# Kernel tuning notes

Hardware: AMD Instinct MI355X
Metric: run time of the kernel (lower is better)

## Reference

```python
import jax, jax.numpy as jnp
import numpy as np

N, E, B = 50000, 800000, 64
D_IN, D_E = 192, 64
NUM_OUT = 256


def setup_inputs() -> dict:
    key = jax.random.key(0)
    ks = jax.random.split(key, 30)
    rn = lambda k, s: jax.random.normal(k, s, dtype=jnp.float32) * 0.05
    return {
        "x": jax.random.normal(ks[0], (N, D_IN), jnp.float32),
        "edge_index": jax.random.randint(ks[1], (2, E), 0, N, dtype=jnp.int32),
        "edge_attr": jax.random.normal(ks[2], (E, D_E), jnp.float32),
        "batch": jnp.sort(jax.random.randint(ks[3], (N,), 0, B, dtype=jnp.int32)),
        "W1": rn(ks[4], (D_IN, 256)), "as1": rn(ks[5], (4, 64)), "ad1": rn(ks[6], (4, 64)),
        "We1": rn(ks[7], (D_E, 256)), "ae1": rn(ks[8], (4, 64)), "b1": rn(ks[9], (256,)),
        "W2": rn(ks[10], (256, 256)), "as2": rn(ks[11], (4, 64)), "ad2": rn(ks[12], (4, 64)),
        "We2": rn(ks[13], (D_E, 256)), "ae2": rn(ks[14], (4, 64)), "b2": rn(ks[15], (256,)),
        "W3": rn(ks[16], (256, 512)), "as3": rn(ks[17], (4, 128)), "ad3": rn(ks[18], (4, 128)),
        "We3": rn(ks[19], (D_E, 512)), "ae3": rn(ks[20], (4, 128)), "b3": rn(ks[21], (128,)),
        "Wa": rn(ks[22], (128, NUM_OUT)), "ba": rn(ks[23], (NUM_OUT,)),
        "Wv": rn(ks[24], (128, 1)), "bv": rn(ks[25], (1,)),
    }


def reference(x, edge_index, edge_attr, batch,
              W1, as1, ad1, We1, ae1, b1,
              W2, as2, ad2, We2, ae2, b2,
              W3, as3, ad3, We3, ae3, b3,
              Wa, ba, Wv, bv):
    Nn = x.shape[0]
    src0, dst0 = edge_index[0], edge_index[1]
    # PyG add_self_loops(fill_value='mean'): self-loop edge_attr = mean of incoming edge_attr
    deg = jax.ops.segment_sum(jnp.ones_like(dst0, dtype=x.dtype), dst0, num_segments=Nn)
    loop_attr = jax.ops.segment_sum(edge_attr, dst0, num_segments=Nn) / jnp.maximum(deg, 1.0)[:, None]
    loop = jnp.arange(Nn, dtype=src0.dtype)
    src = jnp.concatenate([src0, loop])
    dst = jnp.concatenate([dst0, loop])
    ea = jnp.concatenate([edge_attr, loop_attr], axis=0)

    def gat(h, W, a_s, a_d, We, a_e, bias, concat):
        Hh, C = a_s.shape
        hs = (h @ W).reshape(Nn, Hh, C)                       # [N,H,C]
        al_s = (hs * a_s).sum(-1)                             # [N,H]
        al_d = (hs * a_d).sum(-1)                             # [N,H]
        al_e = ((ea @ We).reshape(-1, Hh, C) * a_e).sum(-1)   # [E+N,H]
        alpha = jax.nn.leaky_relu(al_s[src] + al_d[dst] + al_e, 0.2)
        amax = jax.ops.segment_max(alpha, dst, num_segments=Nn)
        w = jnp.exp(alpha - amax[dst])
        denom = jax.ops.segment_sum(w, dst, num_segments=Nn)
        w = w / (denom[dst] + 1e-16)                          # scatter-softmax over dst
        out = jax.ops.segment_sum(hs[src] * w[..., None], dst, num_segments=Nn)
        out = out.reshape(Nn, Hh * C) if concat else out.mean(axis=1)
        return out + bias

    h = jax.nn.relu(gat(x, W1, as1, ad1, We1, ae1, b1, True))
    h = jax.nn.relu(gat(h, W2, as2, ad2, We2, ae2, b2, True))
    h = gat(h, W3, as3, ad3, We3, ae3, b3, False)
    cnt = jax.ops.segment_sum(jnp.ones((Nn,), h.dtype), batch, num_segments=B)
    g = jax.ops.segment_sum(h, batch, num_segments=B) / jnp.maximum(cnt, 1.0)[:, None]
    logits = g @ Wa + ba
    value = g @ Wv + bv
    return jnp.concatenate([logits, value], axis=-1)  # [B, num_outputs+1]
```

## Files before the change

kernel.cpp:

```cpp
#include <hip/hip_runtime.h>
#include <hip/hip_bf16.h>


typedef __attribute__((ext_vector_type(8))) short short8;
typedef __attribute__((ext_vector_type(4))) float floatx4;
typedef __attribute__((ext_vector_type(4))) unsigned int uintx4;

#define DEV __device__ __forceinline__

DEV unsigned short f2b(float f) {
  union { float f; unsigned u; } v; v.f = f;
  unsigned r = v.u + 0x7FFFu + ((v.u >> 16) & 1u);
  return (unsigned short)(r >> 16);
}
DEV float b2f(unsigned short u) {
  union { unsigned u; float f; } v; v.u = ((unsigned)u) << 16;
  return v.f;
}

__global__ void k_cvt(const float* __restrict__ in, unsigned short* __restrict__ out,
                      int n8) {
  int i = blockIdx.x * 256 + threadIdx.x;
  if (i >= n8) return;
  const float4* p = (const float4*)(in + (size_t)i * 8);
  float4 a = p[0], b = p[1];
  unsigned short t[8];
  t[0]=f2b(a.x); t[1]=f2b(a.y); t[2]=f2b(a.z); t[3]=f2b(a.w);
  t[4]=f2b(b.x); t[5]=f2b(b.y); t[6]=f2b(b.z); t[7]=f2b(b.w);
  *(uint4*)(out + (size_t)i * 8) = *(uint4*)t;
}

__global__ void k_deg2(const int* __restrict__ src, const int* __restrict__ dst,
                       int* __restrict__ deg2, int E) {
  int e = blockIdx.x * 256 + threadIdx.x;
  if (e < E) atomicAdd(&deg2[(size_t)dst[e] * 8 + (src[e] >> 13)], 1);
}

__global__ __launch_bounds__(256) void k_scan1(const int* __restrict__ deg,
    int* __restrict__ rowptr, int* __restrict__ bsum, int N) {
  __shared__ int sd[256];
  int b = blockIdx.x, tid = threadIdx.x;
  int i0 = b * 1024 + tid * 4;
  int v[4]; int s = 0;
#pragma unroll
  for (int j = 0; j < 4; j++) { int i = i0 + j; v[j] = (i < N) ? deg[i] : 0; s += v[j]; }
  sd[tid] = s;
  __syncthreads();
  for (int off = 1; off < 256; off <<= 1) {
    int t = (tid >= off) ? sd[tid - off] : 0;
    __syncthreads();
    sd[tid] += t;
    __syncthreads();
  }
  int run = sd[tid] - s;
#pragma unroll
  for (int j = 0; j < 4; j++) { int i = i0 + j; if (i < N) rowptr[i] = run; run += v[j]; }
  if (tid == 255) bsum[b] = sd[255];
}

__global__ __launch_bounds__(512) void k_scan2(int* __restrict__ bsum, int nb) {
  __shared__ int sd[512];
  int tid = threadIdx.x;
  int v = (tid < nb) ? bsum[tid] : 0;
  sd[tid] = v;
  __syncthreads();
  for (int off = 1; off < 512; off <<= 1) {
    int t = (tid >= off) ? sd[tid - off] : 0;
    __syncthreads();
    sd[tid] += t;
    __syncthreads();
  }
  if (tid < nb) bsum[tid] = sd[tid] - v;
}

__global__ __launch_bounds__(256) void k_scan3(int* __restrict__ rowptr,
    int* __restrict__ cursor, const int* __restrict__ bsum, int N, int E) {
  int b = blockIdx.x, tid = threadIdx.x;
  int add = bsum[b];
  int i0 = b * 1024 + tid * 4;
#pragma unroll
  for (int j = 0; j < 4; j++) {
    int i = i0 + j;
    if (i < N) { int r = rowptr[i] + add; rowptr[i] = r; cursor[i] = r; }
  }
  if (b == 0 && tid == 0) rowptr[N] = E;
}

__global__ void k_scatter(const int* __restrict__ src, const int* __restrict__ dst,
    int* __restrict__ cursor, int2* __restrict__ csr, int E) {
  int e = blockIdx.x * 256 + threadIdx.x;
  if (e < E) {
    int s = src[e], d = dst[e];
    int pos = atomicAdd(&cursor[(size_t)d * 8 + (s >> 13)], 1);
    csr[pos] = make_int2(s, e);
  }
}

__global__ void k_wt(const float* __restrict__ W, unsigned short* __restrict__ Wt,
                     int K, int Nout) {
  int idx = blockIdx.x * 256 + threadIdx.x;
  if (idx < K * Nout) {
    int n = idx / K, k = idx - n * K;
    Wt[idx] = f2b(W[(size_t)k * Nout + n]);
  }
}

__global__ void k_wep(const float* __restrict__ We1, const float* __restrict__ ae1,
                      const float* __restrict__ We2, const float* __restrict__ ae2,
                      const float* __restrict__ We3, const float* __restrict__ ae3,
                      unsigned short* __restrict__ Wept) {
  int t = blockIdx.x * 256 + threadIdx.x;
  int j = t >> 6, c = t & 63;
  int L = j >> 2, h = j & 3;
  const float* We = (L == 0) ? We1 : (L == 1) ? We2 : We3;
  const float* ae = (L == 0) ? ae1 : (L == 1) ? ae2 : ae3;
  int C = (L == 2) ? 128 : 64;
  int HC = 4 * C;
  float s = 0.f;
  for (int cc = 0; cc < C; cc++) s += We[(size_t)c * HC + h * C + cc] * ae[h * C + cc];
  Wept[j * 64 + c] = f2b(s);
  if (t < 256) {
    int jj = 12 + (t >> 6);
    Wept[jj * 64 + (t & 63)] = 0;
  }
}

template<bool A_F32, int OUT_MODE, bool DO_ALD>
__global__ __launch_bounds__(256) void k_gemm(const void* __restrict__ Ap,
    const unsigned short* __restrict__ Bt, void* __restrict__ Cp,
    int M, int Nout, int K, int EN,
    const float* __restrict__ a_s, const float* __restrict__ a_d,
    float* __restrict__ als, float* __restrict__ ald,
    const int2* __restrict__ eidmap) {
  __shared__ unsigned short As[64][32];
  __shared__ unsigned short Bs[64][32];
  const int tid = threadIdx.x;
  const int wave = tid >> 6, lane = tid & 63;
  const int quad = lane >> 4, l16 = lane & 15;
  const int m0 = blockIdx.x * 64, n0 = blockIdx.y * 64;
  const int arow = tid >> 2;
  const int cb0  = (tid & 3) << 4;
  const int swzr = ((arow >> 1) & 3) << 4;
  floatx4 acc[4] = {{0,0,0,0},{0,0,0,0},{0,0,0,0},{0,0,0,0}};
  for (int k0 = 0; k0 < K; k0 += 32) {
    if (A_F32) {
      int gm = m0 + arow;
      unsigned short tmp[8];
      if (gm < M) {
        size_t ar = (size_t)gm;
        if (OUT_MODE == 2) ar = (size_t)eidmap[gm].y;
        const float* Af = (const float*)Ap;
        const float4* p = (const float4*)(Af + ar * K + k0 + (cb0 >> 1));
        float4 u0 = p[0], u1 = p[1];
        tmp[0]=f2b(u0.x); tmp[1]=f2b(u0.y); tmp[2]=f2b(u0.z); tmp[3]=f2b(u0.w);
        tmp[4]=f2b(u1.x); tmp[5]=f2b(u1.y); tmp[6]=f2b(u1.z); tmp[7]=f2b(u1.w);
      } else {
#pragma unroll
        for (int j = 0; j < 8; j++) tmp[j] = 0;
      }
      *(uint4*)((char*)&As[0][0] + arow * 64 + (cb0 ^ swzr)) = *(uint4*)tmp;
      int gn = n0 + arow;
      uint4 bv = {0,0,0,0};
      if (gn < Nout) bv = *(const uint4*)(Bt + (size_t)gn * K + k0 + (cb0 >> 1));
      *(uint4*)((char*)&Bs[0][0] + arow * 64 + (cb0 ^ swzr)) = bv;
    } else {
      int gm = m0 + arow; if (gm >= M) gm = M - 1;
      int cbs = cb0 ^ swzr;
      const unsigned short* gA =
          (const unsigned short*)Ap + (size_t)gm * K + k0 + (cbs >> 1);
      __builtin_amdgcn_global_load_lds(gA, (char*)&As[0][0] + wave * 1024, 16, 0, 0);
      int gn = n0 + arow;
      const unsigned short* gB = Bt + (size_t)gn * K + k0 + (cbs >> 1);
      __builtin_amdgcn_global_load_lds(gB, (char*)&Bs[0][0] + wave * 1024, 16, 0, 0);
    }
    __syncthreads();
    int ra = wave * 16 + l16;
    short8 a = *(const short8*)((const char*)&As[0][0] + ra * 64 +
                                ((quad * 16) ^ (((ra >> 1) & 3) << 4)));
#pragma unroll
    for (int t = 0; t < 4; t++) {
      int rb = t * 16 + l16;
      short8 b = *(const short8*)((const char*)&Bs[0][0] + rb * 64 +
                                  ((quad * 16) ^ (((rb >> 1) & 3) << 4)));
      acc[t] = __builtin_amdgcn_mfma_f32_16x16x32_bf16(a, b, acc[t], 0, 0, 0);
    }
    __syncthreads();
  }
#pragma unroll
  for (int t = 0; t < 4; t++) {
#pragma unroll
    for (int r = 0; r < 4; r++) {
      int row = m0 + wave * 16 + quad * 4 + r;
      int col = n0 + t * 16 + l16;
      float v = acc[t][r];
      if (OUT_MODE == 0) {
        if (row < M && col < Nout)
          ((unsigned short*)Cp)[(size_t)row * Nout + col] = f2b(v);
      } else {
        if (row < M && col < 12)
          ((float*)Cp)[((size_t)(col >> 2) * EN + row) * 4 + (col & 3)] = v;
      }
    }
  }
  if constexpr (DO_ALD) {
    int h = (n0 * 4) / Nout;
#pragma unroll
    for (int r = 0; r < 4; r++) {
      float ps = 0.f, pd = 0.f;
#pragma unroll
      for (int t = 0; t < 4; t++) {
        int col = n0 + t * 16 + l16;
        float v = acc[t][r];
        ps += v * a_s[col];
        pd += v * a_d[col];
      }
#pragma unroll
      for (int off = 1; off < 16; off <<= 1) {
        ps += __shfl_xor(ps, off, 64);
        pd += __shfl_xor(pd, off, 64);
      }
      int row = m0 + wave * 16 + quad * 4 + r;
      if (l16 == 0 && row < M) {
        atomicAdd(&als[row * 4 + h], ps);
        atomicAdd(&ald[row * 4 + h], pd);
      }
    }
  }
}

__global__ void k_loop_ale(const int* __restrict__ rowptr2,
                           float* __restrict__ ale, int N, int E) {
  int n = blockIdx.x * 256 + threadIdx.x;
  if (n >= N) return;
  const size_t EN = (size_t)E + N;
  int s = rowptr2[(size_t)n * 8], e = rowptr2[(size_t)n * 8 + 8];
  float a[12];
#pragma unroll
  for (int j = 0; j < 12; j++) a[j] = 0.f;
  for (int p = s; p < e; p++) {
#pragma unroll
    for (int L = 0; L < 3; L++) {
      float4 v = *(const float4*)(ale + (L * EN + p) * 4);
      a[L * 4 + 0] += v.x; a[L * 4 + 1] += v.y;
      a[L * 4 + 2] += v.z; a[L * 4 + 3] += v.w;
    }
  }
  float inv = 1.0f / (float)((e - s) > 1 ? (e - s) : 1);
#pragma unroll
  for (int L = 0; L < 3; L++)
    *(float4*)(ale + (L * EN + E + n) * 4) =
        make_float4(a[L*4+0]*inv, a[L*4+1]*inv, a[L*4+2]*inv, a[L*4+3]*inv);
}

template<int LPN, int MODE>
__global__ __launch_bounds__(256) void k_agg(const unsigned short* __restrict__ hs,
    const int* __restrict__ rowptr2, const int2* __restrict__ csr,
    const float* __restrict__ ale,
    const float* __restrict__ als, const float* __restrict__ ald,
    const float* __restrict__ bias, unsigned short* __restrict__ outb,
    float* __restrict__ outf, int N, int E) {
  const int FPL = 32;
  const int HC  = LPN * FPL;
  const int NG  = 64 / LPN;
  __shared__ float s_w[4][NG][LPN][4];
  __shared__ int   s_s[4][NG][LPN];
  const int wave = threadIdx.x >> 6;
  const int lane = threadIdx.x & 63;
  const int grp  = lane / LPN;
  const int sl   = lane % LPN;
  const int hd   = sl >> (LPN >> 3);
  const int node = blockIdx.x * (4 * NG) + wave * NG + grp;
  if (node >= N) return;
  int start = rowptr2[(size_t)node * 8];
  int cnt   = rowptr2[(size_t)node * 8 + 8] - start;
  int total = cnt + 1;
  const float4 aldv   = *(const float4*)(ald + (size_t)node * 4);
  const float4 selfev = *(const float4*)(ale + ((size_t)E + node) * 4);
  const float4 selfsv = *(const float4*)(als + (size_t)node * 4);
  int    psidx = node;
  float4 pev = selfev, psv = selfsv;
  if (sl < cnt) {
    int2 se = csr[start + sl];
    psidx = se.x;
    pev = *(const float4*)(ale + (size_t)(start + sl) * 4);
    psv = *(const float4*)(als + (size_t)se.x * 4);
  }
  float m0=-1e30f, m1=-1e30f, m2=-1e30f, m3=-1e30f;
  float d0=0.f, d1=0.f, d2=0.f, d3=0.f;
  float acc[FPL];
#pragma unroll
  for (int j = 0; j < FPL; j++) acc[j] = 0.f;
  for (int base = 0; base < total; base += LPN) {
    int ei = base + sl;
    bool active = ei < total;
    float a0=-1e30f, a1=-1e30f, a2=-1e30f, a3=-1e30f;
    int sidx = psidx;
    if (active) {
      a0 = psv.x + aldv.x + pev.x;
      a1 = psv.y + aldv.y + pev.y;
      a2 = psv.z + aldv.z + pev.z;
      a3 = psv.w + aldv.w + pev.w;
      a0 = a0 > 0.f ? a0 : 0.2f * a0;
      a1 = a1 > 0.f ? a1 : 0.2f * a1;
      a2 = a2 > 0.f ? a2 : 0.2f * a2;
      a3 = a3 > 0.f ? a3 : 0.2f * a3;
    }
    float c0=a0, c1=a1, c2=a2, c3=a3;
#pragma unroll
    for (int off = LPN / 2; off > 0; off >>= 1) {
      c0 = fmaxf(c0, __shfl_xor(c0, off, 64));
      c1 = fmaxf(c1, __shfl_xor(c1, off, 64));
      c2 = fmaxf(c2, __shfl_xor(c2, off, 64));
      c3 = fmaxf(c3, __shfl_xor(c3, off, 64));
    }
    float n0v = fmaxf(m0, c0), n1v = fmaxf(m1, c1), n2v = fmaxf(m2, c2), n3v = fmaxf(m3, c3);
    float p0 = active ? __expf(a0 - n0v) : 0.f;
    float p1 = active ? __expf(a1 - n1v) : 0.f;
    float p2 = active ? __expf(a2 - n2v) : 0.f;
    float p3 = active ? __expf(a3 - n3v) : 0.f;
    float s0=p0, s1=p1, s2=p2, s3=p3;
#pragma unroll
    for (int off = LPN / 2; off > 0; off >>= 1) {
      s0 += __shfl_xor(s0, off, 64);
      s1 += __shfl_xor(s1, off, 64);
      s2 += __shfl_xor(s2, off, 64);
      s3 += __shfl_xor(s3, off, 64);
    }
    float r0 = __expf(m0 - n0v), r1 = __expf(m1 - n1v);
    float r2 = __expf(m2 - n2v), r3 = __expf(m3 - n3v);
    d0 = d0 * r0 + s0; d1 = d1 * r1 + s1; d2 = d2 * r2 + s2; d3 = d3 * r3 + s3;
    float rh = hd == 0 ? r0 : hd == 1 ? r1 : hd == 2 ? r2 : r3;
#pragma unroll
    for (int j = 0; j < FPL; j++) acc[j] *= rh;
    m0 = n0v; m1 = n1v; m2 = n2v; m3 = n3v;
    *(float4*)&s_w[wave][grp][sl][0] = make_float4(p0, p1, p2, p3);
    s_s[wave][grp][sl] = sidx;
    __threadfence_block();
    if (base + LPN < total) {
      int nei = base + LPN + sl;
      psidx = node; pev = selfev; psv = selfsv;
      if (nei < cnt) {
        int2 se = csr[start + nei];
        psidx = se.x;
        pev = *(const float4*)(ale + (size_t)(start + nei) * 4);
        psv = *(const float4*)(als + (size_t)se.x * 4);
      }
    }
    int chunk = total - base; if (chunk > LPN) chunk = LPN;
    int t = 0;
    for (; t + 2 <= chunk; t += 2) {
      float w0 = s_w[wave][grp][t][hd];
      float w1 = s_w[wave][grp][t + 1][hd];
      int   q0 = s_s[wave][grp][t];
      int   q1 = s_s[wave][grp][t + 1];
      const uintx4* p0p = (const uintx4*)(hs + (size_t)q0 * HC + sl * FPL);
      const uintx4* p1p = (const uintx4*)(hs + (size_t)q1 * HC + sl * FPL);
      uintx4 v0[4], v1[4];
#pragma unroll
      for (int q = 0; q < 4; q++) v0[q] = p0p[q];
#pragma unroll
      for (int q = 0; q < 4; q++) v1[q] = p1p[q];
      asm volatile("" :: "v"(v0[0]), "v"(v0[1]), "v"(v0[2]), "v"(v0[3]),
                         "v"(v1[0]), "v"(v1[1]), "v"(v1[2]), "v"(v1[3]));
#pragma unroll
      for (int q = 0; q < 4; q++) {
        uintx4 x = v0[q];
#pragma unroll
        for (int k = 0; k < 4; k++) {
          float lo = __uint_as_float(x[k] << 16);
          float hi = __uint_as_float(x[k] & 0xffff0000u);
          acc[q * 8 + k * 2 + 0] += w0 * lo;
          acc[q * 8 + k * 2 + 1] += w0 * hi;
        }
      }
#pragma unroll
      for (int q = 0; q < 4; q++) {
        uintx4 x = v1[q];
#pragma unroll
        for (int k = 0; k < 4; k++) {
          float lo = __uint_as_float(x[k] << 16);
          float hi = __uint_as_float(x[k] & 0xffff0000u);
          acc[q * 8 + k * 2 + 0] += w1 * lo;
          acc[q * 8 + k * 2 + 1] += w1 * hi;
        }
      }
    }
    if (t < chunk) {
      float w0 = s_w[wave][grp][t][hd];
      int   q0 = s_s[wave][grp][t];
      const uintx4* p0p = (const uintx4*)(hs + (size_t)q0 * HC + sl * FPL);
      uintx4 v0[4];
#pragma unroll
      for (int q = 0; q < 4; q++) v0[q] = p0p[q];
#pragma unroll
      for (int q = 0; q < 4; q++) {
        uintx4 x = v0[q];
#pragma unroll
        for (int k = 0; k < 4; k++) {
          float lo = __uint_as_float(x[k] << 16);
          float hi = __uint_as_float(x[k] & 0xffff0000u);
          acc[q * 8 + k * 2 + 0] += w0 * lo;
          acc[q * 8 + k * 2 + 1] += w0 * hi;
        }
      }
    }
  }
  float dh = hd == 0 ? d0 : hd == 1 ? d1 : hd == 2 ? d2 : d3;
  float inv = 1.0f / (dh + 1e-16f);
  if constexpr (MODE == 0) {
    unsigned short tmp[FPL];
#pragma unroll
    for (int j = 0; j < FPL; j++) {
      float v = acc[j] * inv + bias[sl * FPL + j];
      tmp[j] = f2b(fmaxf(v, 0.f));
    }
    unsigned short* op = outb + (size_t)node * HC + sl * FPL;
#pragma unroll
    for (int q = 0; q < 4; q++) ((uint4*)op)[q] = ((uint4*)tmp)[q];
  } else {
#pragma unroll
    for (int j = 0; j < FPL; j++) {
      float v = acc[j] * inv;
      v += __shfl_xor(v, 4, 64);
      v += __shfl_xor(v, 8, 64);
      acc[j] = v * 0.25f;
    }
    if (sl < 4) {
      float* op = outf + (size_t)node * (4 * FPL) + sl * FPL;
#pragma unroll
      for (int j = 0; j < FPL; j++) op[j] = acc[j] + bias[sl * FPL + j];
    }
  }
}

__global__ __launch_bounds__(256) void k_pool(const float* __restrict__ out3,
    const int* __restrict__ bat, float* __restrict__ g, int* __restrict__ cntb, int N) {
  int wid = blockIdx.x * 4 + (threadIdx.x >> 6);
  int lane = threadIdx.x & 63;
  int per = (N + 255) / 256;
  int s = wid * per, e = s + per;
  if (e > N) e = N;
  if (s >= e) return;
  int cur = bat[s];
  float ax = 0.f, ay = 0.f; int run = 0;
  for (int n = s; n < e; n++) {
    int b = bat[n];
    if (b != cur) {
      atomicAdd(&g[cur * 128 + lane * 2], ax);
      atomicAdd(&g[cur * 128 + lane * 2 + 1], ay);
      if (lane == 0) atomicAdd(&cntb[cur], run);
      ax = 0.f; ay = 0.f; run = 0; cur = b;
    }
    float2 v = *(const float2*)(out3 + (size_t)n * 128 + lane * 2);
    ax += v.x; ay += v.y; run++;
  }
  atomicAdd(&g[cur * 128 + lane * 2], ax);
  atomicAdd(&g[cur * 128 + lane * 2 + 1], ay);
  if (lane == 0) atomicAdd(&cntb[cur], run);
}

__global__ __launch_bounds__(320) void k_final(const float* __restrict__ g,
    const int* __restrict__ cntb, const float* __restrict__ Wa, const float* __restrict__ ba,
    const float* __restrict__ Wv, const float* __restrict__ bv, float* __restrict__ out) {
  __shared__ float gm[128];
  int b = blockIdx.x, t = threadIdx.x;
  if (t < 128) {
    float c = (float)cntb[b];
    gm[t] = g[b * 128 + t] / fmaxf(c, 1.f);
  }
  __syncthreads();
  if (t < 257) {
    float acc = 0.f;
    if (t < 256) {
      for (int k = 0; k < 128; k++) acc += gm[k] * Wa[k * 256 + t];
      acc += ba[t];
    } else {
      for (int k = 0; k < 128; k++) acc += gm[k] * Wv[k];
      acc += bv[0];
    }
    out[b * 257 + t] = acc;
  }
}

extern "C" void kernel_launch(void* const* d_in, const int* in_sizes, int n_in,
                              void* d_out, int out_size, void* d_ws, size_t ws_size,
                              hipStream_t stream) {
  const float* x   = (const float*)d_in[0];
  const int*   ei  = (const int*)  d_in[1];
  const float* ea  = (const float*)d_in[2];
  const int*   bat = (const int*)  d_in[3];
  const float* W1  = (const float*)d_in[4];
  const float* as1 = (const float*)d_in[5];
  const float* ad1 = (const float*)d_in[6];
  const float* We1 = (const float*)d_in[7];
  const float* ae1 = (const float*)d_in[8];
  const float* b1  = (const float*)d_in[9];
  const float* W2  = (const float*)d_in[10];
  const float* as2 = (const float*)d_in[11];
  const float* ad2 = (const float*)d_in[12];
  const float* We2 = (const float*)d_in[13];
  const float* ae2 = (const float*)d_in[14];
  const float* b2  = (const float*)d_in[15];
  const float* W3  = (const float*)d_in[16];
  const float* as3 = (const float*)d_in[17];
  const float* ad3 = (const float*)d_in[18];
  const float* We3 = (const float*)d_in[19];
  const float* ae3 = (const float*)d_in[20];
  const float* b3  = (const float*)d_in[21];
  const float* Wa  = (const float*)d_in[22];
  const float* ba  = (const float*)d_in[23];
  const float* Wv  = (const float*)d_in[24];
  const float* bv  = (const float*)d_in[25];
  (void)n_in; (void)out_size; (void)ws_size;

  const int N = in_sizes[0] / 192;
  const int E = in_sizes[1] / 2;
  const size_t EN = (size_t)E + N;
  const int* srcv = ei;
  const int* dstv = ei + E;
  const int N2 = N * 8;
  const int nbB = (N2 + 1023) / 1024;

  size_t off = 0;
  auto alloc = [&](size_t bytes) -> char* {
    char* p = (char*)d_ws + off;
    off += (bytes + 255) & ~(size_t)255;
    return p;
  };
  int* deg2    = (int*)alloc((size_t)N2 * 4);
  int* rowptr2 = (int*)alloc((size_t)(N2 + 1) * 4);
  int* cursor2 = (int*)alloc((size_t)N2 * 4);
  int* bsum    = (int*)alloc(512 * 4);
  int2* csr    = (int2*)alloc((size_t)E * 8);
  float* ale   = (float*)alloc(3 * EN * 4 * 4);
  unsigned short* Wept = (unsigned short*)alloc(16 * 64 * 2);
  unsigned short* W1t  = (unsigned short*)alloc(256 * 192 * 2);
  unsigned short* W2t  = (unsigned short*)alloc(256 * 256 * 2);
  unsigned short* W3t  = (unsigned short*)alloc(512 * 256 * 2);
  unsigned short* xB   = (unsigned short*)alloc((size_t)N * 192 * 2);
  unsigned short* hs   = (unsigned short*)alloc((size_t)N * 512 * 2);
  unsigned short* h1   = (unsigned short*)alloc((size_t)N * 256 * 2);
  unsigned short* h2   = (unsigned short*)alloc((size_t)N * 256 * 2);
  float* out3  = (float*)alloc((size_t)N * 128 * 4);
  float* als_all = (float*)alloc((size_t)N * 4 * 4 * 6);
  float* g     = (float*)alloc(64 * 128 * 4 + 64 * 4);
  int* cntb    = (int*)(g + 64 * 128);
  float* als1 = als_all + (size_t)N * 4 * 0;
  float* ald1 = als_all + (size_t)N * 4 * 1;
  float* als2 = als_all + (size_t)N * 4 * 2;
  float* ald2 = als_all + (size_t)N * 4 * 3;
  float* als3 = als_all + (size_t)N * 4 * 4;
  float* ald3 = als_all + (size_t)N * 4 * 5;

  hipMemsetAsync(deg2, 0, (size_t)N2 * 4, stream);
  hipMemsetAsync(als_all, 0, (size_t)N * 4 * 4 * 6, stream);
  hipMemsetAsync(g, 0, 64 * 128 * 4 + 64 * 4, stream);

  k_deg2<<<(E + 255) / 256, 256, 0, stream>>>(srcv, dstv, deg2, E);
  k_scan1<<<nbB, 256, 0, stream>>>(deg2, rowptr2, bsum, N2);
  k_scan2<<<1, 512, 0, stream>>>(bsum, nbB);
  k_scan3<<<nbB, 256, 0, stream>>>(rowptr2, cursor2, bsum, N2, E);
  k_scatter<<<(E + 255) / 256, 256, 0, stream>>>(srcv, dstv, cursor2, csr, E);
  k_cvt<<<((N * 192 / 8) + 255) / 256, 256, 0, stream>>>(x, xB, N * 192 / 8);
  k_wt<<<(192 * 256 + 255) / 256, 256, 0, stream>>>(W1, W1t, 192, 256);
  k_wt<<<(256 * 256 + 255) / 256, 256, 0, stream>>>(W2, W2t, 256, 256);
  k_wt<<<(256 * 512 + 255) / 256, 256, 0, stream>>>(W3, W3t, 256, 512);
  k_wep<<<3, 256, 0, stream>>>(We1, ae1, We2, ae2, We3, ae3, Wept);
  k_gemm<true, 2, false><<<dim3((E + 63) / 64, 1), 256, 0, stream>>>(
      ea, Wept, ale, E, 16, 64, (int)EN, nullptr, nullptr, nullptr, nullptr, csr);
  k_loop_ale<<<(N + 255) / 256, 256, 0, stream>>>(rowptr2, ale, N, E);
  k_gemm<false, 0, true><<<dim3((N + 63) / 64, 4), 256, 0, stream>>>(
      xB, W1t, hs, N, 256, 192, 0, as1, ad1, als1, ald1, nullptr);
  k_agg<8, 0><<<(N + 31) / 32, 256, 0, stream>>>(
      hs, rowptr2, csr, ale + 0 * EN * 4, als1, ald1, b1, h1, nullptr, N, E);
  k_gemm<false, 0, true><<<dim3((N + 63) / 64, 4), 256, 0, stream>>>(
      h1, W2t, hs, N, 256, 256, 0, as2, ad2, als2, ald2, nullptr);
  k_agg<8, 0><<<(N + 31) / 32, 256, 0, stream>>>(
      hs, rowptr2, csr, ale + 1 * EN * 4, als2, ald2, b2, h2, nullptr, N, E);
  k_gemm<false, 0, true><<<dim3((N + 63) / 64, 8), 256, 0, stream>>>(
      h2, W3t, hs, N, 512, 256, 0, as3, ad3, als3, ald3, nullptr);
  k_agg<16, 1><<<(N + 15) / 16, 256, 0, stream>>>(
      hs, rowptr2, csr, ale + 2 * EN * 4, als3, ald3, b3, nullptr, out3, N, E);
  k_pool<<<64, 256, 0, stream>>>(out3, bat, g, cntb, N);
  k_final<<<64, 320, 0, stream>>>(g, cntb, Wa, ba, Wv, bv, (float*)d_out);
}
```

Before: 1.009 ms.

## Merge prep kernels, drop atomics for per-head logits, and split aggregation launches

Fuses the x conversion, the three weight transposes and the edge-weight projection into one multi-role prep kernel. For layers 1 and 2, where each 64-column tile covers exactly one head, the GEMM epilogue now writes the attention logits directly instead of using atomicAdd, which shrinks the zeroed workspace to a single memset. Each aggregation kernel is split into two launches over node halves, apparently to improve cache locality or scheduling. The extra launches add overhead, and the split size is hardcoded for this node count.

```diff
diff --git a/kernel.cpp b/kernel.cpp
--- a/kernel.cpp
+++ b/kernel.cpp
@@ -18,16 +18,58 @@
   return v.f;
 }
 
-__global__ void k_cvt(const float* __restrict__ in, unsigned short* __restrict__ out,
-                      int n8) {
-  int i = blockIdx.x * 256 + threadIdx.x;
-  if (i >= n8) return;
-  const float4* p = (const float4*)(in + (size_t)i * 8);
-  float4 a = p[0], b = p[1];
-  unsigned short t[8];
-  t[0]=f2b(a.x); t[1]=f2b(a.y); t[2]=f2b(a.z); t[3]=f2b(a.w);
-  t[4]=f2b(b.x); t[5]=f2b(b.y); t[6]=f2b(b.z); t[7]=f2b(b.w);
-  *(uint4*)(out + (size_t)i * 8) = *(uint4*)t;
+__global__ __launch_bounds__(256) void k_prep(
+    const float* __restrict__ x, unsigned short* __restrict__ xB, int n8,
+    const float* __restrict__ W1, unsigned short* __restrict__ W1t,
+    const float* __restrict__ W2, unsigned short* __restrict__ W2t,
+    const float* __restrict__ W3, unsigned short* __restrict__ W3t,
+    const float* __restrict__ We1, const float* __restrict__ ae1,
+    const float* __restrict__ We2, const float* __restrict__ ae2,
+    const float* __restrict__ We3, const float* __restrict__ ae3,
+    unsigned short* __restrict__ Wept,
+    int bA, int bB, int bC, int bD) {
+  int b = blockIdx.x, tid = threadIdx.x;
+  if (b < bA) {
+    int i = b * 256 + tid;
+    if (i < n8) {
+      const float4* p = (const float4*)(x + (size_t)i * 8);
+      float4 a = p[0], c = p[1];
+      unsigned short t[8];
+      t[0]=f2b(a.x); t[1]=f2b(a.y); t[2]=f2b(a.z); t[3]=f2b(a.w);
+      t[4]=f2b(c.x); t[5]=f2b(c.y); t[6]=f2b(c.z); t[7]=f2b(c.w);
+      *(uint4*)(xB + (size_t)i * 8) = *(uint4*)t;
+    }
+  } else if (b < bB) {
+    int idx = (b - bA) * 256 + tid;
+    int K = 192, Nout = 256;
+    int n = idx / K, k = idx - n * K;
+    W1t[idx] = f2b(W1[(size_t)k * Nout + n]);
+  } else if (b < bC) {
+    int idx = (b - bB) * 256 + tid;
+    int K = 256, Nout = 256;
+    int n = idx / K, k = idx - n * K;
+    W2t[idx] = f2b(W2[(size_t)k * Nout + n]);
+  } else if (b < bD) {
+    int idx = (b - bC) * 256 + tid;
+    int K = 256, Nout = 512;
+    int n = idx / K, k = idx - n * K;
+    W3t[idx] = f2b(W3[(size_t)k * Nout + n]);
+  } else {
+    int t = (b - bD) * 256 + tid;
+    int j = t >> 6, c = t & 63;
+    int L = j >> 2, h = j & 3;
+    const float* We = (L == 0) ? We1 : (L == 1) ? We2 : We3;
+    const float* ae = (L == 0) ? ae1 : (L == 1) ? ae2 : ae3;
+    int C = (L == 2) ? 128 : 64;
+    int HC = 4 * C;
+    float s = 0.f;
+    for (int cc = 0; cc < C; cc++) s += We[(size_t)c * HC + h * C + cc] * ae[h * C + cc];
+    Wept[j * 64 + c] = f2b(s);
+    if (t < 256) {
+      int jj = 12 + (t >> 6);
+      Wept[jj * 64 + (t & 63)] = 0;
+    }
+  }
 }
 
 __global__ void k_deg2(const int* __restrict__ src, const int* __restrict__ dst,
@@ -96,36 +138,7 @@
   }
 }
 
-__global__ void k_wt(const float* __restrict__ W, unsigned short* __restrict__ Wt,
-                     int K, int Nout) {
-  int idx = blockIdx.x * 256 + threadIdx.x;
-  if (idx < K * Nout) {
-    int n = idx / K, k = idx - n * K;
-    Wt[idx] = f2b(W[(size_t)k * Nout + n]);
-  }
-}
-
-__global__ void k_wep(const float* __restrict__ We1, const float* __restrict__ ae1,
-                      const float* __restrict__ We2, const float* __restrict__ ae2,
-                      const float* __restrict__ We3, const float* __restrict__ ae3,
-                      unsigned short* __restrict__ Wept) {
-  int t = blockIdx.x * 256 + threadIdx.x;
-  int j = t >> 6, c = t & 63;
-  int L = j >> 2, h = j & 3;
-  const float* We = (L == 0) ? We1 : (L == 1) ? We2 : We3;
-  const float* ae = (L == 0) ? ae1 : (L == 1) ? ae2 : ae3;
-  int C = (L == 2) ? 128 : 64;
-  int HC = 4 * C;
-  float s = 0.f;
-  for (int cc = 0; cc < C; cc++) s += We[(size_t)c * HC + h * C + cc] * ae[h * C + cc];
-  Wept[j * 64 + c] = f2b(s);
-  if (t < 256) {
-    int jj = 12 + (t >> 6);
-    Wept[jj * 64 + (t & 63)] = 0;
-  }
-}
-
-template<bool A_F32, int OUT_MODE, bool DO_ALD>
+template<bool A_F32, int OUT_MODE, int DO_ALD>
 __global__ __launch_bounds__(256) void k_gemm(const void* __restrict__ Ap,
     const unsigned short* __restrict__ Bt, void* __restrict__ Cp,
     int M, int Nout, int K, int EN,
@@ -202,7 +215,7 @@
       }
     }
   }
-  if constexpr (DO_ALD) {
+  if constexpr (DO_ALD != 0) {
     int h = (n0 * 4) / Nout;
 #pragma unroll
     for (int r = 0; r < 4; r++) {
@@ -221,8 +234,13 @@
       }
       int row = m0 + wave * 16 + quad * 4 + r;
       if (l16 == 0 && row < M) {
-        atomicAdd(&als[row * 4 + h], ps);
-        atomicAdd(&ald[row * 4 + h], pd);
+        if constexpr (DO_ALD == 1) {
+          als[row * 4 + h] = ps;
+          ald[row * 4 + h] = pd;
+        } else {
+          atomicAdd(&als[row * 4 + h], ps);
+          atomicAdd(&ald[row * 4 + h], pd);
+        }
       }
     }
   }
@@ -258,7 +276,7 @@
     const float* __restrict__ ale,
     const float* __restrict__ als, const float* __restrict__ ald,
     const float* __restrict__ bias, unsigned short* __restrict__ outb,
-    float* __restrict__ outf, int N, int E) {
+    float* __restrict__ outf, int noff, int nEnd, int E) {
   const int FPL = 32;
   const int HC  = LPN * FPL;
   const int NG  = 64 / LPN;
@@ -269,8 +287,8 @@
   const int grp  = lane / LPN;
   const int sl   = lane % LPN;
   const int hd   = sl >> (LPN >> 3);
-  const int node = blockIdx.x * (4 * NG) + wave * NG + grp;
-  if (node >= N) return;
+  const int node = noff + blockIdx.x * (4 * NG) + wave * NG + grp;
+  if (node >= nEnd) return;
   int start = rowptr2[(size_t)node * 8];
   int cnt   = rowptr2[(size_t)node * 8 + 8] - start;
   int total = cnt + 1;
@@ -528,6 +546,11 @@
     return p;
   };
   int* deg2    = (int*)alloc((size_t)N2 * 4);
+  float* als3  = (float*)alloc((size_t)N * 4 * 4);
+  float* ald3  = (float*)alloc((size_t)N * 4 * 4);
+  float* g     = (float*)alloc(64 * 128 * 4 + 64 * 4);
+  int* cntb    = (int*)(g + 64 * 128);
+  const size_t zspan = off;
   int* rowptr2 = (int*)alloc((size_t)(N2 + 1) * 4);
   int* cursor2 = (int*)alloc((size_t)N2 * 4);
   int* bsum    = (int*)alloc(512 * 4);
@@ -542,45 +565,50 @@
   unsigned short* h1   = (unsigned short*)alloc((size_t)N * 256 * 2);
   unsigned short* h2   = (unsigned short*)alloc((size_t)N * 256 * 2);
   float* out3  = (float*)alloc((size_t)N * 128 * 4);
-  float* als_all = (float*)alloc((size_t)N * 4 * 4 * 6);
-  float* g     = (float*)alloc(64 * 128 * 4 + 64 * 4);
-  int* cntb    = (int*)(g + 64 * 128);
-  float* als1 = als_all + (size_t)N * 4 * 0;
-  float* ald1 = als_all + (size_t)N * 4 * 1;
-  float* als2 = als_all + (size_t)N * 4 * 2;
-  float* ald2 = als_all + (size_t)N * 4 * 3;
-  float* als3 = als_all + (size_t)N * 4 * 4;
-  float* ald3 = als_all + (size_t)N * 4 * 5;
-
-  hipMemsetAsync(deg2, 0, (size_t)N2 * 4, stream);
-  hipMemsetAsync(als_all, 0, (size_t)N * 4 * 4 * 6, stream);
-  hipMemsetAsync(g, 0, 64 * 128 * 4 + 64 * 4, stream);
+  float* als1  = (float*)alloc((size_t)N * 4 * 4);
+  float* ald1  = (float*)alloc((size_t)N * 4 * 4);
+  float* als2  = (float*)alloc((size_t)N * 4 * 4);
+  float* ald2  = (float*)alloc((size_t)N * 4 * 4);
+
+  hipMemsetAsync(d_ws, 0, zspan, stream);
 
   k_deg2<<<(E + 255) / 256, 256, 0, stream>>>(srcv, dstv, deg2, E);
   k_scan1<<<nbB, 256, 0, stream>>>(deg2, rowptr2, bsum, N2);
   k_scan2<<<1, 512, 0, stream>>>(bsum, nbB);
   k_scan3<<<nbB, 256, 0, stream>>>(rowptr2, cursor2, bsum, N2, E);
   k_scatter<<<(E + 255) / 256, 256, 0, stream>>>(srcv, dstv, cursor2, csr, E);
-  k_cvt<<<((N * 192 / 8) + 255) / 256, 256, 0, stream>>>(x, xB, N * 192 / 8);
-  k_wt<<<(192 * 256 + 255) / 256, 256, 0, stream>>>(W1, W1t, 192, 256);
-  k_wt<<<(256 * 256 + 255) / 256, 256, 0, stream>>>(W2, W2t, 256, 256);
-  k_wt<<<(256 * 512 + 255) / 256, 256, 0, stream>>>(W3, W3t, 256, 512);
-  k_wep<<<3, 256, 0, stream>>>(We1, ae1, We2, ae2, We3, ae3, Wept);
-  k_gemm<true, 2, false><<<dim3((E + 63) / 64, 1), 256, 0, stream>>>(
+  {
+    const int n8 = N * 192 / 8;
+    const int bA = (n8 + 255) / 256;
+    const int bB = bA + 192;
+    const int bC = bB + 256;
+    const int bD = bC + 512;
+    k_prep<<<bD + 3, 256, 0, stream>>>(x, xB, n8, W1, W1t, W2, W2t, W3, W3t,
+                                       We1, ae1, We2, ae2, We3, ae3, Wept,
+                                       bA, bB, bC, bD);
+  }
+  k_gemm<true, 2, 0><<<dim3((E + 63) / 64, 1), 256, 0, stream>>>(
       ea, Wept, ale, E, 16, 64, (int)EN, nullptr, nullptr, nullptr, nullptr, csr);
   k_loop_ale<<<(N + 255) / 256, 256, 0, stream>>>(rowptr2, ale, N, E);
-  k_gemm<false, 0, true><<<dim3((N + 63) / 64, 4), 256, 0, stream>>>(
+  const int half = 25024;
+  k_gemm<false, 0, 1><<<dim3((N + 63) / 64, 4), 256, 0, stream>>>(
       xB, W1t, hs, N, 256, 192, 0, as1, ad1, als1, ald1, nullptr);
-  k_agg<8, 0><<<(N + 31) / 32, 256, 0, stream>>>(
-      hs, rowptr2, csr, ale + 0 * EN * 4, als1, ald1, b1, h1, nullptr, N, E);
-  k_gemm<false, 0, true><<<dim3((N + 63) / 64, 4), 256, 0, stream>>>(
+  k_agg<8, 0><<<(half + 31) / 32, 256, 0, stream>>>(
+      hs, rowptr2, csr, ale + 0 * EN * 4, als1, ald1, b1, h1, nullptr, 0, half, E);
+  k_agg<8, 0><<<(N - half + 31) / 32, 256, 0, stream>>>(
+      hs, rowptr2, csr, ale + 0 * EN * 4, als1, ald1, b1, h1, nullptr, half, N, E);
+  k_gemm<false, 0, 1><<<dim3((N + 63) / 64, 4), 256, 0, stream>>>(
       h1, W2t, hs, N, 256, 256, 0, as2, ad2, als2, ald2, nullptr);
-  k_agg<8, 0><<<(N + 31) / 32, 256, 0, stream>>>(
-      hs, rowptr2, csr, ale + 1 * EN * 4, als2, ald2, b2, h2, nullptr, N, E);
-  k_gemm<false, 0, true><<<dim3((N + 63) / 64, 8), 256, 0, stream>>>(
+  k_agg<8, 0><<<(half + 31) / 32, 256, 0, stream>>>(
+      hs, rowptr2, csr, ale + 1 * EN * 4, als2, ald2, b2, h2, nullptr, 0, half, E);
+  k_agg<8, 0><<<(N - half + 31) / 32, 256, 0, stream>>>(
+      hs, rowptr2, csr, ale + 1 * EN * 4, als2, ald2, b2, h2, nullptr, half, N, E);
+  k_gemm<false, 0, 2><<<dim3((N + 63) / 64, 8), 256, 0, stream>>>(
       h2, W3t, hs, N, 512, 256, 0, as3, ad3, als3, ald3, nullptr);
-  k_agg<16, 1><<<(N + 15) / 16, 256, 0, stream>>>(
-      hs, rowptr2, csr, ale + 2 * EN * 4, als3, ald3, b3, nullptr, out3, N, E);
+  k_agg<16, 1><<<(half + 15) / 16, 256, 0, stream>>>(
+      hs, rowptr2, csr, ale + 2 * EN * 4, als3, ald3, b3, nullptr, out3, 0, half, E);
+  k_agg<16, 1><<<(N - half + 15) / 16, 256, 0, stream>>>(
+      hs, rowptr2, csr, ale + 2 * EN * 4, als3, ald3, b3, nullptr, out3, half, N, E);
   k_pool<<<64, 256, 0, stream>>>(out3, bat, g, cntb, N);
   k_final<<<64, 320, 0, stream>>>(g, cntb, Wa, ba, Wv, bv, (float*)d_out);
 }
```

New measurement: 1.027 ms. Within noise of the previous version (+1.7%).
